# Kernel tuning notes

Measured on AMD Instinct MI355X. Metric: run time of the kernel, lower is better.

## Reference

```python
import jax, jax.numpy as jnp
import numpy as np

IN_DIM, HID, OUT, N_EXTRA, NTASKS, BATCH = 1024, 2048, 10, 3, 10, 4096
LOGSTD_MEAN, LOGSTD_STD = -6.0, 0.1


def setup_inputs() -> dict:
    key = jax.random.key(0)
    ks = jax.random.split(key, 20)
    n = lambda k, s: jax.random.normal(k, s, dtype=jnp.float32)
    return {
        "x": n(ks[0], (BATCH, IN_DIM)),
        # shared layer 0 (in_dim -> hidden)
        "mu_w0": n(ks[1], (HID, IN_DIM)) * (1.0 / np.sqrt(IN_DIM)),
        "ls_w0": LOGSTD_MEAN + LOGSTD_STD * n(ks[2], (HID, IN_DIM)),
        "mu_b0": n(ks[3], (HID,)) * 0.01,
        "ls_b0": LOGSTD_MEAN + LOGSTD_STD * n(ks[4], (HID,)),
        # shared layers 1..3 (hidden -> hidden), stacked
        "mu_w": n(ks[5], (N_EXTRA, HID, HID)) * (1.0 / np.sqrt(HID)),
        "ls_w": LOGSTD_MEAN + LOGSTD_STD * n(ks[6], (N_EXTRA, HID, HID)),
        "mu_b": n(ks[7], (N_EXTRA, HID)) * 0.01,
        "ls_b": LOGSTD_MEAN + LOGSTD_STD * n(ks[8], (N_EXTRA, HID)),
        # per-task heads (hidden -> out), stacked over tasks
        "mu_hw": n(ks[9], (NTASKS, OUT, HID)) * (1.0 / np.sqrt(HID)),
        "ls_hw": LOGSTD_MEAN + LOGSTD_STD * n(ks[10], (NTASKS, OUT, HID)),
        "mu_hb": n(ks[11], (NTASKS, OUT)) * 0.01,
        "ls_hb": LOGSTD_MEAN + LOGSTD_STD * n(ks[12], (NTASKS, OUT)),
        # reparameterization noise (one sample per forward, as in torch module)
        "eps_w0": n(ks[13], (HID, IN_DIM)),
        "eps_b0": n(ks[14], (HID,)),
        "eps_w": n(ks[15], (N_EXTRA, HID, HID)),
        "eps_b": n(ks[16], (N_EXTRA, HID)),
        "eps_hw": n(ks[17], (NTASKS, OUT, HID)),
        "eps_hb": n(ks[18], (NTASKS, OUT)),
        "task": jax.random.randint(ks[19], (BATCH,), 0, NTASKS, dtype=jnp.int64),
    }


def reference(x, mu_w0, ls_w0, mu_b0, ls_b0, mu_w, ls_w, mu_b, ls_b,
              mu_hw, ls_hw, mu_hb, ls_hb,
              eps_w0, eps_b0, eps_w, eps_b, eps_hw, eps_hb, task):
    # BayesianLinear: w = mu + exp(log_sigma) * eps
    w0 = mu_w0 + jnp.exp(ls_w0) * eps_w0          # [HID, IN]
    b0 = mu_b0 + jnp.exp(ls_b0) * eps_b0          # [HID]
    h = jax.nn.relu(x @ w0.T + b0)                # [B, HID]
    for i in range(N_EXTRA):                      # fixed small layer loop
        wi = mu_w[i] + jnp.exp(ls_w[i]) * eps_w[i]
        bi = mu_b[i] + jnp.exp(ls_b[i]) * eps_b[i]
        h = jax.nn.relu(h @ wi.T + bi)
    # multihead: compute every head, zero out non-matching rows (dense masked)
    hw = mu_hw + jnp.exp(ls_hw) * eps_hw          # [T, OUT, HID]
    hb = mu_hb + jnp.exp(ls_hb) * eps_hb          # [T, OUT]
    out_all = jnp.einsum('bh,toh->bto', h, hw) + hb[None]   # [B, T, OUT]
    onehot = (task[:, None] == jnp.arange(NTASKS)[None, :]).astype(h.dtype)
    return jnp.einsum('bto,bt->bo', out_all, onehot)        # [B, OUT]
```

## Files before the change

kernel.cpp:

```cpp
#include <hip/hip_runtime.h>
#include <cstdint>

#define BATCH 4096
#define IN_DIM 1024
#define HID 2048
#define OUT_DIM 10
#define NTASKS 10

typedef __bf16 bf16x8 __attribute__((ext_vector_type(8)));
typedef float f32x4 __attribute__((ext_vector_type(4)));
typedef __attribute__((address_space(3))) uint8_t lds_u8;
typedef const __attribute__((address_space(1))) uint8_t glb_u8;

__device__ __forceinline__ unsigned short f2bf(float f) {
    uint32_t u = __builtin_bit_cast(uint32_t, f);
    u += 0x7fffu + ((u >> 16) & 1u);
    return (unsigned short)(u >> 16);
}
__device__ __forceinline__ float bf2f(unsigned short h) {
    uint32_t u = ((uint32_t)h) << 16;
    return __builtin_bit_cast(float, u);
}
__device__ __forceinline__ uint32_t pk(float a, float b) {
    return (uint32_t)f2bf(a) | ((uint32_t)f2bf(b) << 16);
}


__global__ __launch_bounds__(256) void bl_transform(
    const float4* __restrict__ mu, const float4* __restrict__ ls,
    const float4* __restrict__ eps, uint4* __restrict__ out)
{
    const int t  = threadIdx.x;
    const int fb = blockIdx.x * 1024;
    const int ia = fb + 2 * t;
    const int ib = fb + 512 + 2 * t;
    const float4 m0 = mu[ia], m1 = mu[ia + 1], m2 = mu[ib], m3 = mu[ib + 1];
    const float4 l0 = ls[ia], l1 = ls[ia + 1], l2 = ls[ib], l3 = ls[ib + 1];
    const float4 e0 = eps[ia], e1 = eps[ia + 1], e2 = eps[ib], e3 = eps[ib + 1];
    uint4 o0, o1;
    o0.x = pk(m0.x + __expf(l0.x) * e0.x, m0.y + __expf(l0.y) * e0.y);
    o0.y = pk(m0.z + __expf(l0.z) * e0.z, m0.w + __expf(l0.w) * e0.w);
    o0.z = pk(m1.x + __expf(l1.x) * e1.x, m1.y + __expf(l1.y) * e1.y);
    o0.w = pk(m1.z + __expf(l1.z) * e1.z, m1.w + __expf(l1.w) * e1.w);
    o1.x = pk(m2.x + __expf(l2.x) * e2.x, m2.y + __expf(l2.y) * e2.y);
    o1.y = pk(m2.z + __expf(l2.z) * e2.z, m2.w + __expf(l2.w) * e2.w);
    o1.z = pk(m3.x + __expf(l3.x) * e3.x, m3.y + __expf(l3.y) * e3.y);
    o1.w = pk(m3.z + __expf(l3.z) * e3.z, m3.w + __expf(l3.w) * e3.w);
    out[blockIdx.x * 512 + t]       = o0;
    out[blockIdx.x * 512 + 256 + t] = o1;
}

__global__ __launch_bounds__(256) void bl_cvt(
    const float4* __restrict__ in, uint4* __restrict__ out)
{
    const int t  = threadIdx.x;
    const int fb = blockIdx.x * 1024;
    const int ia = fb + 2 * t;
    const int ib = fb + 512 + 2 * t;
    const float4 v0 = in[ia], v1 = in[ia + 1], v2 = in[ib], v3 = in[ib + 1];
    uint4 o0, o1;
    o0.x = pk(v0.x, v0.y); o0.y = pk(v0.z, v0.w);
    o0.z = pk(v1.x, v1.y); o0.w = pk(v1.z, v1.w);
    o1.x = pk(v2.x, v2.y); o1.y = pk(v2.z, v2.w);
    o1.z = pk(v3.x, v3.y); o1.w = pk(v3.z, v3.w);
    out[blockIdx.x * 512 + t]       = o0;
    out[blockIdx.x * 512 + 256 + t] = o1;
}

__global__ __launch_bounds__(256) void bl_small(
    const float* __restrict__ mu_b0, const float* __restrict__ ls_b0, const float* __restrict__ eps_b0,
    const float* __restrict__ mu_b,  const float* __restrict__ ls_b,  const float* __restrict__ eps_b,
    const float* __restrict__ mu_hb, const float* __restrict__ ls_hb, const float* __restrict__ eps_hb,
    float* __restrict__ b_all, float* __restrict__ hb)
{
    const int total = 4 * HID + NTASKS * OUT_DIM;
    const int i = blockIdx.x * blockDim.x + threadIdx.x;
    if (i >= total) return;
    if (i < HID) {
        b_all[i] = mu_b0[i] + __expf(ls_b0[i]) * eps_b0[i];
    } else if (i < 4 * HID) {
        const int j = i - HID;
        b_all[HID + j] = mu_b[j] + __expf(ls_b[j]) * eps_b[j];
    } else {
        const int j = i - 4 * HID;
        hb[j] = mu_hb[j] + __expf(ls_hb[j]) * eps_hb[j];
    }
}

#define BAR()        asm volatile("s_barrier" ::: "memory")
#define WAIT_LGKM0() do { asm volatile("s_waitcnt lgkmcnt(0)" ::: "memory"); __builtin_amdgcn_sched_barrier(0); } while (0)
#define RD_A(m, o)   (*(const bf16x8*)(ldsb + acur + (o) + (m)*2048))
#define RD_B(n, o)   (*(const bf16x8*)(ldsb + bcur + (o) + (n)*2048))
#define MFMA(d, va, vb) d = __builtin_amdgcn_mfma_f32_16x16x32_bf16(va, vb, d, 0, 0, 0)
#define STAGEI(i, kel, sl) \
    __builtin_amdgcn_global_load_lds((glb_u8*)(gsrc[i] + (kel)), \
        (lds_u8*)(ldsb + ldst[i] + (uint32_t)(sl) * smul[i]), 16, 0, 0)

template <int UPG, int TMODE>
__global__ __launch_bounds__(640, 1) void bl_gemm(
    const unsigned short* __restrict__ A,
    const unsigned short* __restrict__ B,
    const float* __restrict__ bias,
    unsigned short* __restrict__ C,
    int K,
    const float* __restrict__ tmu, const float* __restrict__ tls,
    const float* __restrict__ teps, void* __restrict__ tdst)
{
    __shared__ unsigned short lds[49152];
    uint8_t* ldsb = (uint8_t*)lds;

    const int tid  = threadIdx.x;
    const int wave = tid >> 6;
    const int lane = tid & 63;
    const int NT = K >> 6;

    if (wave < 8) {
        const int swz = ((blockIdx.x & 7) << 5) | (blockIdx.x >> 3);
        const int bm = swz >> 4;
        const int bn = swz & 15;
        const int wr = wave >> 1;
        const int wc = wave & 1;

        const int lr8 = lane >> 3;
        const int ss  = (lane & 7) ^ lr8;
        const unsigned short* gsrc[6];
        uint32_t ldst[6], smul[6];
        #pragma unroll
        for (int i = 0; i < 6; ++i) {
            const int c = wave * 6 + i;
            if (c < 32) {
                gsrc[i] = A + (size_t)(bm * 256 + c * 8 + lr8) * K + ss * 8;
                ldst[i] = (uint32_t)c * 1024u;
                smul[i] = 32768u;
            } else {
                gsrc[i] = B + (size_t)(bn * 128 + (c - 32) * 8 + lr8) * K + ss * 8;
                ldst[i] = 65536u + (uint32_t)(c - 32) * 1024u;
                smul[i] = 16384u;
            }
        }

        const int rA = wr * 64 + (lane & 15);
        const int rB = wc * 64 + (lane & 15);
        const int ks = lane >> 4;
        const uint32_t aoff0 = (uint32_t)(rA * 128 + ((ks       ^ (rA & 7)) * 16));
        const uint32_t aoff1 = (uint32_t)(rA * 128 + (((4 | ks) ^ (rA & 7)) * 16));
        const uint32_t boff0 = (uint32_t)(rB * 128 + ((ks       ^ (rB & 7)) * 16));
        const uint32_t boff1 = (uint32_t)(rB * 128 + (((4 | ks) ^ (rB & 7)) * 16));

        f32x4 acc[4][4] = {};

        STAGEI(0, 0, 0); STAGEI(1, 0, 0); STAGEI(2, 0, 0);
        STAGEI(3, 0, 0); STAGEI(4, 0, 0); STAGEI(5, 0, 0);
        __syncthreads();

        for (int t = 0; t < NT; ++t) {
            const int cur = t & 1, nxt = cur ^ 1;
            const uint32_t acur = (uint32_t)cur * 32768u;
            const uint32_t bcur = 65536u + (uint32_t)cur * 16384u;
            const bool pf = (t + 1 < NT);
            const int ktn = (t + 1) << 6;

            bf16x8 a0, a1, a2, a3, b0, b1, b2, b3;

            a0 = RD_A(0, aoff0); a1 = RD_A(1, aoff0);
            b0 = RD_B(0, boff0); b1 = RD_B(1, boff0); b2 = RD_B(2, boff0); b3 = RD_B(3, boff0);
            if (pf) { STAGEI(0, ktn, nxt); STAGEI(1, ktn, nxt); STAGEI(2, ktn, nxt); }
            BAR(); WAIT_LGKM0();
            __builtin_amdgcn_s_setprio(1);
            MFMA(acc[0][0], a0, b0); MFMA(acc[0][1], a0, b1); MFMA(acc[0][2], a0, b2); MFMA(acc[0][3], a0, b3);
            MFMA(acc[1][0], a1, b0); MFMA(acc[1][1], a1, b1); MFMA(acc[1][2], a1, b2); MFMA(acc[1][3], a1, b3);
            __builtin_amdgcn_s_setprio(0);
            BAR();

            a2 = RD_A(2, aoff0); a3 = RD_A(3, aoff0);
            if (pf) { STAGEI(3, ktn, nxt); STAGEI(4, ktn, nxt); STAGEI(5, ktn, nxt); }
            BAR(); WAIT_LGKM0();
            __builtin_amdgcn_s_setprio(1);
            MFMA(acc[2][0], a2, b0); MFMA(acc[2][1], a2, b1); MFMA(acc[2][2], a2, b2); MFMA(acc[2][3], a2, b3);
            MFMA(acc[3][0], a3, b0); MFMA(acc[3][1], a3, b1); MFMA(acc[3][2], a3, b2); MFMA(acc[3][3], a3, b3);
            __builtin_amdgcn_s_setprio(0);
            BAR();

            a0 = RD_A(0, aoff1); a1 = RD_A(1, aoff1);
            b0 = RD_B(0, boff1); b1 = RD_B(1, boff1); b2 = RD_B(2, boff1); b3 = RD_B(3, boff1);
            BAR(); WAIT_LGKM0();
            __builtin_amdgcn_s_setprio(1);
            MFMA(acc[0][0], a0, b0); MFMA(acc[0][1], a0, b1); MFMA(acc[0][2], a0, b2); MFMA(acc[0][3], a0, b3);
            MFMA(acc[1][0], a1, b0); MFMA(acc[1][1], a1, b1); MFMA(acc[1][2], a1, b2); MFMA(acc[1][3], a1, b3);
            __builtin_amdgcn_s_setprio(0);
            BAR();

            a2 = RD_A(2, aoff1); a3 = RD_A(3, aoff1);
            BAR(); WAIT_LGKM0();
            __builtin_amdgcn_s_setprio(1);
            MFMA(acc[2][0], a2, b0); MFMA(acc[2][1], a2, b1); MFMA(acc[2][2], a2, b2); MFMA(acc[2][3], a2, b3);
            MFMA(acc[3][0], a3, b0); MFMA(acc[3][1], a3, b1); MFMA(acc[3][2], a3, b2); MFMA(acc[3][3], a3, b3);
            __builtin_amdgcn_s_setprio(0);
            __syncthreads();
        }

        const int col0 = bn * 128 + wc * 64 + (lane & 15);
        const int row0 = bm * 256 + wr * 64 + ((lane >> 4) << 2);
        #pragma unroll
        for (int n = 0; n < 4; ++n) {
            const int col = col0 + n * 16;
            const float bv = bias[col];
            #pragma unroll
            for (int m = 0; m < 4; ++m) {
                #pragma unroll
                for (int j = 0; j < 4; ++j) {
                    float v = acc[m][n][j] + bv;
                    v = v > 0.0f ? v : 0.0f;
                    C[(size_t)(row0 + m * 16 + j) * HID + col] = f2bf(v);
                }
            }
        }
    } else {
        const int tw = tid - 512;
        const float4* m4 = (const float4*)tmu;
        const float4* l4 = (const float4*)tls;
        const float4* e4 = (const float4*)teps;

        float4 pm[UPG], pl[UPG], pe[UPG];
        size_t base;
        if (TMODE == 0) {
            base = (size_t)blockIdx.x * 4096;
            #pragma unroll
            for (int q = 0; q < UPG; ++q) {
                const size_t g = base + (size_t)q * 128 + tw;
                pm[q] = m4[g]; pl[q] = l4[g]; pe[q] = e4[g];
            }
        } else {
            base = (size_t)blockIdx.x * 200;
        }
        __syncthreads();

        for (int t = 0; t < NT; ++t) {
            if (TMODE == 0) {
                ushort4* d4 = (ushort4*)tdst;
                #pragma unroll
                for (int q = 0; q < UPG; ++q) {
                    const size_t g = base + ((size_t)t * UPG + q) * 128 + tw;
                    ushort4 r;
                    r.x = f2bf(pm[q].x + __expf(pl[q].x) * pe[q].x);
                    r.y = f2bf(pm[q].y + __expf(pl[q].y) * pe[q].y);
                    r.z = f2bf(pm[q].z + __expf(pl[q].z) * pe[q].z);
                    r.w = f2bf(pm[q].w + __expf(pl[q].w) * pe[q].w);
                    d4[g] = r;
                }
                if (t + 1 < NT) {
                    #pragma unroll
                    for (int q = 0; q < UPG; ++q) {
                        const size_t g2 = base + ((size_t)(t + 1) * UPG + q) * 128 + tw;
                        pm[q] = m4[g2]; pl[q] = l4[g2]; pe[q] = e4[g2];
                    }
                }
            } else {
                const int lo = t * 128 + tw;
                if (lo < 200) {
                    const size_t g = base + lo;
                    const float4 m = m4[g], l = l4[g], e = e4[g];
                    float4 r;
                    r.x = m.x + __expf(l.x) * e.x;
                    r.y = m.y + __expf(l.y) * e.y;
                    r.z = m.z + __expf(l.z) * e.z;
                    r.w = m.w + __expf(l.w) * e.w;
                    ((float4*)tdst)[g] = r;
                }
            }
            BAR(); BAR(); BAR(); BAR(); BAR(); BAR(); BAR();
            __syncthreads();
        }
    }
}

__global__ __launch_bounds__(256) void bl_head(
    const unsigned short* __restrict__ h,
    const float* __restrict__ hw,
    const float* __restrict__ hb,
    const int* __restrict__ task,
    float* __restrict__ out)
{
    const int wave = threadIdx.x >> 6, lane = threadIdx.x & 63;
    const int b = blockIdx.x * 4 + wave;
    const int t = task[b];
    const float* w = hw + (size_t)t * OUT_DIM * HID;
    const unsigned short* hr = h + (size_t)b * HID;

    float acc[OUT_DIM];
    #pragma unroll
    for (int o = 0; o < OUT_DIM; ++o) acc[o] = 0.0f;

    #pragma unroll
    for (int i = 0; i < HID / 512; ++i) {
        const int k0 = (i * 64 + lane) * 8;
        const bf16x8 hv8 = *(const bf16x8*)(hr + k0);
        float hf[8];
        #pragma unroll
        for (int j = 0; j < 8; ++j) hf[j] = (float)hv8[j];
        #pragma unroll
        for (int o = 0; o < OUT_DIM; ++o) {
            const float4 w0 = *(const float4*)(w + (size_t)o * HID + k0);
            const float4 w1 = *(const float4*)(w + (size_t)o * HID + k0 + 4);
            acc[o] += hf[0]*w0.x + hf[1]*w0.y + hf[2]*w0.z + hf[3]*w0.w
                    + hf[4]*w1.x + hf[5]*w1.y + hf[6]*w1.z + hf[7]*w1.w;
        }
    }
    #pragma unroll
    for (int o = 0; o < OUT_DIM; ++o) {
        float v = acc[o];
        #pragma unroll
        for (int s = 32; s > 0; s >>= 1) v += __shfl_down(v, s, 64);
        if (lane == 0) out[(size_t)b * OUT_DIM + o] = v + hb[t * OUT_DIM + o];
    }
}


extern "C" void kernel_launch(void* const* d_in, const int* in_sizes, int n_in,
                              void* d_out, int out_size, void* d_ws, size_t ws_size,
                              hipStream_t stream)
{
    const float* x      = (const float*)d_in[0];
    const float* mu_w0  = (const float*)d_in[1];
    const float* ls_w0  = (const float*)d_in[2];
    const float* mu_b0  = (const float*)d_in[3];
    const float* ls_b0  = (const float*)d_in[4];
    const float* mu_w   = (const float*)d_in[5];
    const float* ls_w   = (const float*)d_in[6];
    const float* mu_b   = (const float*)d_in[7];
    const float* ls_b   = (const float*)d_in[8];
    const float* mu_hw  = (const float*)d_in[9];
    const float* ls_hw  = (const float*)d_in[10];
    const float* mu_hb  = (const float*)d_in[11];
    const float* ls_hb  = (const float*)d_in[12];
    const float* eps_w0 = (const float*)d_in[13];
    const float* eps_b0 = (const float*)d_in[14];
    const float* eps_w  = (const float*)d_in[15];
    const float* eps_b  = (const float*)d_in[16];
    const float* eps_hw = (const float*)d_in[17];
    const float* eps_hb = (const float*)d_in[18];
    const int*   task   = (const int*)d_in[19];

    uint8_t* ws = (uint8_t*)d_ws;
    constexpr size_t HH     = (size_t)HID * HID;
    constexpr size_t X_OFF  = 0;
    constexpr size_t W0_OFF = X_OFF  + (size_t)BATCH * IN_DIM * 2;
    constexpr size_t W_OFF  = W0_OFF + (size_t)HID * IN_DIM * 2;
    constexpr size_t H0_OFF = W_OFF  + 3 * HH * 2;
    constexpr size_t H1_OFF = H0_OFF + (size_t)BATCH * HID * 2;
    constexpr size_t B_OFF  = H1_OFF + (size_t)BATCH * HID * 2;
    constexpr size_t HW_OFF = B_OFF  + (size_t)4 * HID * 4;
    constexpr size_t HB_OFF = HW_OFF + (size_t)NTASKS * OUT_DIM * HID * 4;

    unsigned short* xbf = (unsigned short*)(ws + X_OFF);
    unsigned short* w0b = (unsigned short*)(ws + W0_OFF);
    unsigned short* wb  = (unsigned short*)(ws + W_OFF);
    unsigned short* h0  = (unsigned short*)(ws + H0_OFF);
    unsigned short* h1  = (unsigned short*)(ws + H1_OFF);
    float* ball = (float*)(ws + B_OFF);
    float* hwf  = (float*)(ws + HW_OFF);
    float* hbf  = (float*)(ws + HB_OFF);

    bl_cvt<<<BATCH * IN_DIM / 4096, 256, 0, stream>>>((const float4*)x, (uint4*)xbf);
    bl_transform<<<HID * IN_DIM / 4096, 256, 0, stream>>>(
        (const float4*)mu_w0, (const float4*)ls_w0, (const float4*)eps_w0, (uint4*)w0b);
    bl_small<<<(4 * HID + NTASKS * OUT_DIM + 255) / 256, 256, 0, stream>>>(
        mu_b0, ls_b0, eps_b0, mu_b, ls_b, eps_b, mu_hb, ls_hb, eps_hb, ball, hbf);

    bl_gemm<2, 0><<<256, 640, 0, stream>>>(xbf, w0b, ball, h0, IN_DIM,
        mu_w, ls_w, eps_w, (void*)wb);
    bl_gemm<1, 0><<<256, 640, 0, stream>>>(h0, wb, ball + HID, h1, HID,
        mu_w + HH, ls_w + HH, eps_w + HH, (void*)(wb + HH));
    bl_gemm<1, 0><<<256, 640, 0, stream>>>(h1, wb + HH, ball + 2 * HID, h0, HID,
        mu_w + 2 * HH, ls_w + 2 * HH, eps_w + 2 * HH, (void*)(wb + 2 * HH));
    bl_gemm<1, 1><<<256, 640, 0, stream>>>(h0, wb + 2 * HH, ball + 3 * HID, h1, HID,
        mu_hw, ls_hw, eps_hw, (void*)hwf);

    bl_head<<<BATCH / 4, 256, 0, stream>>>(h1, hwf, hbf, task, (float*)d_out);
}
```

Before: 198.4 us.

## Fuse fp32-to-bf16 conversion of x into first GEMM's A-tile staging

Drops the separate bl_cvt kernel. The first GEMM now loads fp32 x through registers, converts it to bf16 and writes it into LDS, which removes one launch and a full write and re-read of the bf16 copy of x. The helper waves that transform the next layer's weights are also restructured into a double-buffered load/compute/store pipeline. The cost is extra VGPR pressure and register-path loads for A in layer 0, in place of direct global-to-LDS loads.

```diff
diff --git a/kernel.cpp b/kernel.cpp
--- a/kernel.cpp
+++ b/kernel.cpp
@@ -17,14 +17,15 @@
     u += 0x7fffu + ((u >> 16) & 1u);
     return (unsigned short)(u >> 16);
 }
-__device__ __forceinline__ float bf2f(unsigned short h) {
-    uint32_t u = ((uint32_t)h) << 16;
-    return __builtin_bit_cast(float, u);
-}
 __device__ __forceinline__ uint32_t pk(float a, float b) {
     return (uint32_t)f2bf(a) | ((uint32_t)f2bf(b) << 16);
 }
-
+__device__ __forceinline__ uint4 cv8(float4 a, float4 b) {
+    uint4 r;
+    r.x = pk(a.x, a.y); r.y = pk(a.z, a.w);
+    r.z = pk(b.x, b.y); r.w = pk(b.z, b.w);
+    return r;
+}
 
 __global__ __launch_bounds__(256) void bl_transform(
     const float4* __restrict__ mu, const float4* __restrict__ ls,
@@ -50,23 +51,6 @@
     out[blockIdx.x * 512 + 256 + t] = o1;
 }
 
-__global__ __launch_bounds__(256) void bl_cvt(
-    const float4* __restrict__ in, uint4* __restrict__ out)
-{
-    const int t  = threadIdx.x;
-    const int fb = blockIdx.x * 1024;
-    const int ia = fb + 2 * t;
-    const int ib = fb + 512 + 2 * t;
-    const float4 v0 = in[ia], v1 = in[ia + 1], v2 = in[ib], v3 = in[ib + 1];
-    uint4 o0, o1;
-    o0.x = pk(v0.x, v0.y); o0.y = pk(v0.z, v0.w);
-    o0.z = pk(v1.x, v1.y); o0.w = pk(v1.z, v1.w);
-    o1.x = pk(v2.x, v2.y); o1.y = pk(v2.z, v2.w);
-    o1.z = pk(v3.x, v3.y); o1.w = pk(v3.z, v3.w);
-    out[blockIdx.x * 512 + t]       = o0;
-    out[blockIdx.x * 512 + 256 + t] = o1;
-}
-
 __global__ __launch_bounds__(256) void bl_small(
     const float* __restrict__ mu_b0, const float* __restrict__ ls_b0, const float* __restrict__ eps_b0,
     const float* __restrict__ mu_b,  const float* __restrict__ ls_b,  const float* __restrict__ eps_b,
@@ -92,14 +76,11 @@
 #define RD_A(m, o)   (*(const bf16x8*)(ldsb + acur + (o) + (m)*2048))
 #define RD_B(n, o)   (*(const bf16x8*)(ldsb + bcur + (o) + (n)*2048))
 #define MFMA(d, va, vb) d = __builtin_amdgcn_mfma_f32_16x16x32_bf16(va, vb, d, 0, 0, 0)
-#define STAGEI(i, kel, sl) \
-    __builtin_amdgcn_global_load_lds((glb_u8*)(gsrc[i] + (kel)), \
-        (lds_u8*)(ldsb + ldst[i] + (uint32_t)(sl) * smul[i]), 16, 0, 0)
-
-template <int UPG, int TMODE>
+
+template <int UPG, int TMODE, bool AF32>
 __global__ __launch_bounds__(640, 1) void bl_gemm(
-    const unsigned short* __restrict__ A,
-    const unsigned short* __restrict__ B,
+    const void* __restrict__ Ap,
+    const unsigned short* __restrict__ Bw,
     const float* __restrict__ bias,
     unsigned short* __restrict__ C,
     int K,
@@ -116,28 +97,36 @@
 
     if (wave < 8) {
         const int swz = ((blockIdx.x & 7) << 5) | (blockIdx.x >> 3);
-        const int bm = swz >> 4;
-        const int bn = swz & 15;
-        const int wr = wave >> 1;
-        const int wc = wave & 1;
-
+        const int bm = swz >> 4, bn = swz & 15;
+        const int wr = wave >> 1, wc = wave & 1;
         const int lr8 = lane >> 3;
         const int ss  = (lane & 7) ^ lr8;
-        const unsigned short* gsrc[6];
-        uint32_t ldst[6], smul[6];
-        #pragma unroll
-        for (int i = 0; i < 6; ++i) {
-            const int c = wave * 6 + i;
-            if (c < 32) {
-                gsrc[i] = A + (size_t)(bm * 256 + c * 8 + lr8) * K + ss * 8;
-                ldst[i] = (uint32_t)c * 1024u;
-                smul[i] = 32768u;
-            } else {
-                gsrc[i] = B + (size_t)(bn * 128 + (c - 32) * 8 + lr8) * K + ss * 8;
-                ldst[i] = 65536u + (uint32_t)(c - 32) * 1024u;
-                smul[i] = 16384u;
-            }
-        }
+        const int K4  = K >> 2;
+
+        const unsigned short* gA[4];
+        const float4* gAf[4];
+        #pragma unroll
+        for (int i = 0; i < 4; ++i) {
+            const int row = bm * 256 + (wave * 4 + i) * 8 + lr8;
+            if constexpr (AF32) gAf[i] = (const float4*)Ap + (size_t)row * K4 + ss * 2;
+            else                gA[i]  = (const unsigned short*)Ap + (size_t)row * K + ss * 8;
+        }
+        const unsigned short* gB[2];
+        #pragma unroll
+        for (int j = 0; j < 2; ++j) {
+            const int row = bn * 128 + (wave * 2 + j) * 8 + lr8;
+            gB[j] = Bw + (size_t)row * K + ss * 8;
+        }
+        const uint32_t aWD = (uint32_t)(wave * 4) * 1024u + (uint32_t)lane * 16u;
+
+        auto STAGEA = [&](int i, int kel, int sl) {
+            __builtin_amdgcn_global_load_lds((glb_u8*)(gA[i] + kel),
+                (lds_u8*)(ldsb + (uint32_t)(wave * 4 + i) * 1024u + (uint32_t)sl * 32768u), 16, 0, 0);
+        };
+        auto STAGEB = [&](int j, int kel, int sl) {
+            __builtin_amdgcn_global_load_lds((glb_u8*)(gB[j] + kel),
+                (lds_u8*)(ldsb + 65536u + (uint32_t)(wave * 2 + j) * 1024u + (uint32_t)sl * 16384u), 16, 0, 0);
+        };
 
         const int rA = wr * 64 + (lane & 15);
         const int rB = wc * 64 + (lane & 15);
@@ -148,9 +137,19 @@
         const uint32_t boff1 = (uint32_t)(rB * 128 + (((4 | ks) ^ (rB & 7)) * 16));
 
         f32x4 acc[4][4] = {};
-
-        STAGEI(0, 0, 0); STAGEI(1, 0, 0); STAGEI(2, 0, 0);
-        STAGEI(3, 0, 0); STAGEI(4, 0, 0); STAGEI(5, 0, 0);
+        float4 Aa[4], Abv[4];
+
+        if constexpr (AF32) {
+            #pragma unroll
+            for (int i = 0; i < 4; ++i) { Aa[i] = gAf[i][0]; Abv[i] = gAf[i][1]; }
+            STAGEB(0, 0, 0); STAGEB(1, 0, 0);
+            #pragma unroll
+            for (int i = 0; i < 4; ++i)
+                *(uint4*)(ldsb + aWD + (uint32_t)i * 1024u) = cv8(Aa[i], Abv[i]);
+        } else {
+            STAGEA(0, 0, 0); STAGEA(1, 0, 0); STAGEA(2, 0, 0); STAGEA(3, 0, 0);
+            STAGEB(0, 0, 0); STAGEB(1, 0, 0);
+        }
         __syncthreads();
 
         for (int t = 0; t < NT; ++t) {
@@ -159,12 +158,16 @@
             const uint32_t bcur = 65536u + (uint32_t)cur * 16384u;
             const bool pf = (t + 1 < NT);
             const int ktn = (t + 1) << 6;
+            const int k4n = (t + 1) * 16;
 
             bf16x8 a0, a1, a2, a3, b0, b1, b2, b3;
 
             a0 = RD_A(0, aoff0); a1 = RD_A(1, aoff0);
             b0 = RD_B(0, boff0); b1 = RD_B(1, boff0); b2 = RD_B(2, boff0); b3 = RD_B(3, boff0);
-            if (pf) { STAGEI(0, ktn, nxt); STAGEI(1, ktn, nxt); STAGEI(2, ktn, nxt); }
+            if (pf) {
+                STAGEB(0, ktn, nxt); STAGEB(1, ktn, nxt);
+                if constexpr (!AF32) { STAGEA(0, ktn, nxt); }
+            }
             BAR(); WAIT_LGKM0();
             __builtin_amdgcn_s_setprio(1);
             MFMA(acc[0][0], a0, b0); MFMA(acc[0][1], a0, b1); MFMA(acc[0][2], a0, b2); MFMA(acc[0][3], a0, b3);
@@ -173,7 +176,14 @@
             BAR();
 
             a2 = RD_A(2, aoff0); a3 = RD_A(3, aoff0);
-            if (pf) { STAGEI(3, ktn, nxt); STAGEI(4, ktn, nxt); STAGEI(5, ktn, nxt); }
+            if (pf) {
+                if constexpr (AF32) {
+                    #pragma unroll
+                    for (int i = 0; i < 4; ++i) { Aa[i] = gAf[i][k4n]; Abv[i] = gAf[i][k4n + 1]; }
+                } else {
+                    STAGEA(1, ktn, nxt); STAGEA(2, ktn, nxt); STAGEA(3, ktn, nxt);
+                }
+            }
             BAR(); WAIT_LGKM0();
             __builtin_amdgcn_s_setprio(1);
             MFMA(acc[2][0], a2, b0); MFMA(acc[2][1], a2, b1); MFMA(acc[2][2], a2, b2); MFMA(acc[2][3], a2, b3);
@@ -196,6 +206,14 @@
             MFMA(acc[2][0], a2, b0); MFMA(acc[2][1], a2, b1); MFMA(acc[2][2], a2, b2); MFMA(acc[2][3], a2, b3);
             MFMA(acc[3][0], a3, b0); MFMA(acc[3][1], a3, b1); MFMA(acc[3][2], a3, b2); MFMA(acc[3][3], a3, b3);
             __builtin_amdgcn_s_setprio(0);
+            if constexpr (AF32) {
+                if (pf) {
+                    const uint32_t ad = aWD + (uint32_t)nxt * 32768u;
+                    #pragma unroll
+                    for (int i = 0; i < 4; ++i)
+                        *(uint4*)(ldsb + ad + (uint32_t)i * 1024u) = cv8(Aa[i], Abv[i]);
+                }
+            }
             __syncthreads();
         }
 
@@ -217,59 +235,86 @@
         }
     } else {
         const int tw = tid - 512;
-        const float4* m4 = (const float4*)tmu;
-        const float4* l4 = (const float4*)tls;
-        const float4* e4 = (const float4*)teps;
-
-        float4 pm[UPG], pl[UPG], pe[UPG];
-        size_t base;
-        if (TMODE == 0) {
-            base = (size_t)blockIdx.x * 4096;
-            #pragma unroll
-            for (int q = 0; q < UPG; ++q) {
-                const size_t g = base + (size_t)q * 128 + tw;
-                pm[q] = m4[g]; pl[q] = l4[g]; pe[q] = e4[g];
-            }
-        } else {
-            base = (size_t)blockIdx.x * 200;
-        }
-        __syncthreads();
-
-        for (int t = 0; t < NT; ++t) {
-            if (TMODE == 0) {
-                ushort4* d4 = (ushort4*)tdst;
+        if constexpr (TMODE == 0) {
+            const float4* m4 = (const float4*)tmu;
+            const float4* l4 = (const float4*)tls;
+            const float4* e4 = (const float4*)teps;
+            ushort4* d4 = (ushort4*)tdst;
+            const uint32_t base = (uint32_t)blockIdx.x * 4096u + (uint32_t)tw;
+
+            float4 mA[UPG], lA[UPG], eA[UPG], mB[UPG], lB[UPG], eB[UPG];
+            ushort4 rsA[UPG], rsB[UPG];
+
+            auto LD = [&](int t, float4* m, float4* l, float4* e) {
+                if (t < NT) {
+                    #pragma unroll
+                    for (int q = 0; q < UPG; ++q) {
+                        const uint32_t g = base + (uint32_t)(t * UPG + q) * 128u;
+                        m[q] = m4[g]; l[q] = l4[g]; e[q] = e4[g];
+                    }
+                }
+            };
+            auto CP = [&](float4* m, float4* l, float4* e, ushort4* r) {
                 #pragma unroll
                 for (int q = 0; q < UPG; ++q) {
-                    const size_t g = base + ((size_t)t * UPG + q) * 128 + tw;
-                    ushort4 r;
-                    r.x = f2bf(pm[q].x + __expf(pl[q].x) * pe[q].x);
-                    r.y = f2bf(pm[q].y + __expf(pl[q].y) * pe[q].y);
-                    r.z = f2bf(pm[q].z + __expf(pl[q].z) * pe[q].z);
-                    r.w = f2bf(pm[q].w + __expf(pl[q].w) * pe[q].w);
-                    d4[g] = r;
-                }
-                if (t + 1 < NT) {
-                    #pragma unroll
-                    for (int q = 0; q < UPG; ++q) {
-                        const size_t g2 = base + ((size_t)(t + 1) * UPG + q) * 128 + tw;
-                        pm[q] = m4[g2]; pl[q] = l4[g2]; pe[q] = e4[g2];
+                    r[q].x = f2bf(m[q].x + __expf(l[q].x) * e[q].x);
+                    r[q].y = f2bf(m[q].y + __expf(l[q].y) * e[q].y);
+                    r[q].z = f2bf(m[q].z + __expf(l[q].z) * e[q].z);
+                    r[q].w = f2bf(m[q].w + __expf(l[q].w) * e[q].w);
+                }
+            };
+            auto ST = [&](int t, ushort4* r) {
+                #pragma unroll
+                for (int q = 0; q < UPG; ++q)
+                    d4[base + (uint32_t)(t * UPG + q) * 128u] = r[q];
+            };
+
+            LD(0, mA, lA, eA); LD(1, mB, lB, eB);
+            __syncthreads();
+            for (int t = 0; t < NT; t += 2) {
+                if (t > 0) ST(t - 1, rsB);
+                CP(mA, lA, eA, rsA);
+                LD(t + 2, mA, lA, eA);
+                BAR(); BAR(); BAR(); BAR(); BAR(); BAR(); BAR();
+                __syncthreads();
+                ST(t, rsA);
+                CP(mB, lB, eB, rsB);
+                LD(t + 3, mB, lB, eB);
+                BAR(); BAR(); BAR(); BAR(); BAR(); BAR(); BAR();
+                __syncthreads();
+            }
+            ST(NT - 1, rsB);
+        } else {
+            const float4* m4 = (const float4*)tmu;
+            const float4* l4 = (const float4*)tls;
+            const float4* e4 = (const float4*)teps;
+            float4* o4 = (float4*)tdst;
+            const uint32_t b0i = (uint32_t)blockIdx.x * 200u + (uint32_t)tw;
+            float4 m0 = m4[b0i], l0 = l4[b0i], e0 = e4[b0i];
+            float4 m1, l1, e1;
+            if (tw < 72) { m1 = m4[b0i + 128]; l1 = l4[b0i + 128]; e1 = e4[b0i + 128]; }
+            __syncthreads();
+            float4 r0, r1;
+            for (int t = 0; t < NT; ++t) {
+                if (t == 0) {
+                    r0.x = m0.x + __expf(l0.x) * e0.x;
+                    r0.y = m0.y + __expf(l0.y) * e0.y;
+                    r0.z = m0.z + __expf(l0.z) * e0.z;
+                    r0.w = m0.w + __expf(l0.w) * e0.w;
+                    if (tw < 72) {
+                        r1.x = m1.x + __expf(l1.x) * e1.x;
+                        r1.y = m1.y + __expf(l1.y) * e1.y;
+                        r1.z = m1.z + __expf(l1.z) * e1.z;
+                        r1.w = m1.w + __expf(l1.w) * e1.w;
                     }
-                }
-            } else {
-                const int lo = t * 128 + tw;
-                if (lo < 200) {
-                    const size_t g = base + lo;
-                    const float4 m = m4[g], l = l4[g], e = e4[g];
-                    float4 r;
-                    r.x = m.x + __expf(l.x) * e.x;
-                    r.y = m.y + __expf(l.y) * e.y;
-                    r.z = m.z + __expf(l.z) * e.z;
-                    r.w = m.w + __expf(l.w) * e.w;
-                    ((float4*)tdst)[g] = r;
-                }
-            }
-            BAR(); BAR(); BAR(); BAR(); BAR(); BAR(); BAR();
-            __syncthreads();
+                } else if (t == 1) {
+                    o4[b0i] = r0;
+                } else if (t == 2) {
+                    if (tw < 72) o4[b0i + 128] = r1;
+                }
+                BAR(); BAR(); BAR(); BAR(); BAR(); BAR(); BAR();
+                __syncthreads();
+            }
         }
     }
 }
@@ -343,8 +388,7 @@
 
     uint8_t* ws = (uint8_t*)d_ws;
     constexpr size_t HH     = (size_t)HID * HID;
-    constexpr size_t X_OFF  = 0;
-    constexpr size_t W0_OFF = X_OFF  + (size_t)BATCH * IN_DIM * 2;
+    constexpr size_t W0_OFF = 0;
     constexpr size_t W_OFF  = W0_OFF + (size_t)HID * IN_DIM * 2;
     constexpr size_t H0_OFF = W_OFF  + 3 * HH * 2;
     constexpr size_t H1_OFF = H0_OFF + (size_t)BATCH * HID * 2;
@@ -352,7 +396,6 @@
     constexpr size_t HW_OFF = B_OFF  + (size_t)4 * HID * 4;
     constexpr size_t HB_OFF = HW_OFF + (size_t)NTASKS * OUT_DIM * HID * 4;
 
-    unsigned short* xbf = (unsigned short*)(ws + X_OFF);
     unsigned short* w0b = (unsigned short*)(ws + W0_OFF);
     unsigned short* wb  = (unsigned short*)(ws + W_OFF);
     unsigned short* h0  = (unsigned short*)(ws + H0_OFF);
@@ -361,19 +404,21 @@
     float* hwf  = (float*)(ws + HW_OFF);
     float* hbf  = (float*)(ws + HB_OFF);
 
-    bl_cvt<<<BATCH * IN_DIM / 4096, 256, 0, stream>>>((const float4*)x, (uint4*)xbf);
     bl_transform<<<HID * IN_DIM / 4096, 256, 0, stream>>>(
         (const float4*)mu_w0, (const float4*)ls_w0, (const float4*)eps_w0, (uint4*)w0b);
     bl_small<<<(4 * HID + NTASKS * OUT_DIM + 255) / 256, 256, 0, stream>>>(
         mu_b0, ls_b0, eps_b0, mu_b, ls_b, eps_b, mu_hb, ls_hb, eps_hb, ball, hbf);
 
-    bl_gemm<2, 0><<<256, 640, 0, stream>>>(xbf, w0b, ball, h0, IN_DIM,
-        mu_w, ls_w, eps_w, (void*)wb);
-    bl_gemm<1, 0><<<256, 640, 0, stream>>>(h0, wb, ball + HID, h1, HID,
+    bl_gemm<2, 0, true><<<256, 640, 0, stream>>>(
+        x, w0b, ball, h0, IN_DIM, mu_w, ls_w, eps_w, (void*)wb);
+    bl_gemm<1, 0, false><<<256, 640, 0, stream>>>(
+        h0, wb, ball + HID, h1, HID,
         mu_w + HH, ls_w + HH, eps_w + HH, (void*)(wb + HH));
-    bl_gemm<1, 0><<<256, 640, 0, stream>>>(h1, wb + HH, ball + 2 * HID, h0, HID,
+    bl_gemm<1, 0, false><<<256, 640, 0, stream>>>(
+        h1, wb + HH, ball + 2 * HID, h0, HID,
         mu_w + 2 * HH, ls_w + 2 * HH, eps_w + 2 * HH, (void*)(wb + 2 * HH));
-    bl_gemm<1, 1><<<256, 640, 0, stream>>>(h0, wb + 2 * HH, ball + 3 * HID, h1, HID,
+    bl_gemm<1, 1, false><<<256, 640, 0, stream>>>(
+        h0, wb + 2 * HH, ball + 3 * HID, h1, HID,
         mu_hw, ls_hw, eps_hw, (void*)hwf);
 
     bl_head<<<BATCH / 4, 256, 0, stream>>>(h1, hwf, hbf, task, (float*)d_out);
```

New measurement: 247.4 us. 1.25x slower.
